# Kernel optimization log

Measured on AMD Instinct MI355X. Metric: run time of the kernel, lower is better.

## Reference

```python
import jax, jax.numpy as jnp
import numpy as np

N_USERS = 50000
N_DISHES = 10000
N_EDGES = 200000
D_IN = 1024
HID = 256
OUT = 128


def _dense_params(key, d_in, d_out):
    kw, kb = jax.random.split(key)
    W = jax.random.normal(kw, (d_in, d_out), jnp.float32) * (1.0 / np.sqrt(d_in))
    b = jnp.zeros((d_out,), jnp.float32)
    return W, b


def setup_inputs() -> dict:
    key = jax.random.key(0)
    ks = jax.random.split(key, 12)
    inp = {
        "user_feat": jax.random.normal(ks[0], (N_USERS, D_IN), jnp.float32),
        "dish_feat": jax.random.normal(ks[1], (N_DISHES, D_IN), jnp.float32),
        "edge_user": jax.random.randint(ks[2], (N_EDGES,), 0, N_USERS, jnp.int32),
        "edge_dish": jax.random.randint(ks[3], (N_EDGES,), 0, N_DISHES, jnp.int32),
    }
    inp["W_ui"], inp["b_ui"] = _dense_params(ks[4], D_IN, HID)   # user_initial_proj
    inp["W_di"], inp["b_di"] = _dense_params(ks[5], D_IN, HID)   # dish_initial_proj
    inp["W_um"], inp["b_um"] = _dense_params(ks[6], D_IN, HID)   # user_message_fn (sender=dish)
    inp["W_dm"], inp["b_dm"] = _dense_params(ks[7], D_IN, HID)   # dish_message_fn (sender=user)
    inp["W_uu"], inp["b_uu"] = _dense_params(ks[8], HID, HID)    # user_update_fn
    inp["W_du"], inp["b_du"] = _dense_params(ks[9], HID, HID)    # dish_update_fn
    inp["W_up"], inp["b_up"] = _dense_params(ks[10], HID, OUT)   # user_proj
    inp["W_dp"], inp["b_dp"] = _dense_params(ks[11], HID, OUT)   # dish_proj
    return inp


def reference(user_feat, dish_feat, edge_user, edge_dish,
              W_ui, b_ui, W_di, b_di, W_um, b_um, W_dm, b_dm,
              W_uu, b_uu, W_du, b_du, W_up, b_up, W_dp, b_dp):
    # initial projections
    user_init = jax.nn.relu(user_feat @ W_ui + b_ui)   # [U, H]
    dish_init = jax.nn.relu(dish_feat @ W_di + b_di)   # [D, H]

    # SimpleConv on 'interacts_reverse': sender=dish, receiver=user
    u_msg = jax.nn.relu(dish_feat[edge_dish] @ W_um + b_um)          # [E, H]
    user_agg = jax.ops.segment_sum(u_msg, edge_user, num_segments=N_USERS)
    user_upd = jax.nn.relu((user_agg + user_init) @ W_uu + b_uu)
    user_emb = user_upd @ W_up + b_up                                 # [U, OUT]

    # SimpleConv on 'interacts': sender=user, receiver=dish
    d_msg = jax.nn.relu(user_feat[edge_user] @ W_dm + b_dm)          # [E, H]
    dish_agg = jax.ops.segment_sum(d_msg, edge_dish, num_segments=N_DISHES)
    dish_upd = jax.nn.relu((dish_agg + dish_init) @ W_du + b_du)
    dish_emb = dish_upd @ W_dp + b_dp                                 # [D, OUT]

    return (user_emb, dish_emb)
```

## Files before the change

### kernel.cpp

```cpp
#include <hip/hip_runtime.h>
#include <hip/hip_bf16.h>

#define D_IN  1024
#define HID   256
#define OUT_D 128

using bf16x8  = __attribute__((ext_vector_type(8))) short;
using bf16x4  = __attribute__((ext_vector_type(4))) short;
using f32x4   = __attribute__((ext_vector_type(4))) float;
typedef unsigned int u32;

__device__ inline float bf2f(short s) {
    unsigned u = ((unsigned)(unsigned short)s) << 16;
    return __uint_as_float(u);
}
__device__ inline short f2bf(float f) {
    __hip_bfloat16 h = __float2bfloat16(f);
    return *reinterpret_cast<short*>(&h);
}

__device__ __forceinline__ void gld16(void* lds, const void* g) {
    __builtin_amdgcn_global_load_lds(
        (const __attribute__((address_space(1))) u32*)g,
        (__attribute__((address_space(3))) u32*)lds, 16, 0, 0);
}

__global__ void pack_all(
    const float* __restrict__ W_ui, const float* __restrict__ W_dm,
    const float* __restrict__ W_di, const float* __restrict__ W_um,
    const float* __restrict__ W_uu, const float* __restrict__ W_du,
    const float* __restrict__ W_up, const float* __restrict__ W_dp,
    const float* __restrict__ b_ui, const float* __restrict__ b_dm,
    const float* __restrict__ b_di, const float* __restrict__ b_um,
    short* __restrict__ Wut, short* __restrict__ Wdt,
    short* __restrict__ Wuut, short* __restrict__ Wdut,
    short* __restrict__ Wupt, short* __restrict__ Wdpt,
    float* __restrict__ bu, float* __restrict__ bd)
{
    const int z = blockIdx.z;
    const int tx = threadIdx.x, ty = threadIdx.y;
    if (z == 8) {
        if (blockIdx.x != 0 || blockIdx.y != 0) return;
        int t = ty * 32 + tx;
        bu[t] = b_ui[t]; bu[256 + t] = b_dm[t];
        bd[t] = b_di[t]; bd[256 + t] = b_um[t];
        return;
    }
    const float* in; short* out; int K, N, n_off = 0;
    switch (z) {
        case 0: in = W_ui; out = Wut;  K = 1024; N = 256; n_off = 0;   break;
        case 1: in = W_dm; out = Wut;  K = 1024; N = 256; n_off = 256; break;
        case 2: in = W_di; out = Wdt;  K = 1024; N = 256; n_off = 0;   break;
        case 3: in = W_um; out = Wdt;  K = 1024; N = 256; n_off = 256; break;
        case 4: in = W_uu; out = Wuut; K = 256;  N = 256; break;
        case 5: in = W_du; out = Wdut; K = 256;  N = 256; break;
        case 6: in = W_up; out = Wupt; K = 256;  N = 128; break;
        default:in = W_dp; out = Wdpt; K = 256;  N = 128; break;
    }
    const int n0 = blockIdx.x * 32, k0 = blockIdx.y * 32;
    if (n0 >= N || k0 >= K) return;
    __shared__ float t[32][33];
#pragma unroll
    for (int j = 0; j < 32; j += 8)
        t[ty + j][tx] = in[(size_t)(k0 + ty + j) * N + (n0 + tx)];
    __syncthreads();
#pragma unroll
    for (int j = 0; j < 32; j += 8)
        out[(size_t)(n_off + n0 + ty + j) * K + (k0 + tx)] = f2bf(t[tx][ty + j]);
}

template <bool RELU, bool AF32, bool CF32>
__global__ __launch_bounds__(256) void mfma_gemm2(
    const void* __restrict__ A0_, int lda0, const short* __restrict__ Wt0,
    const float* __restrict__ bias0, void* __restrict__ C0,
    int M0, int N0, int K0, int nN0, int nb0,
    const void* __restrict__ A1_, int lda1, const short* __restrict__ Wt1,
    const float* __restrict__ bias1, void* __restrict__ C1,
    int M1, int N1, int K1, int nN1)
{
    constexpr int ABYTES = AF32 ? 16384 : 8192;
    constexpr int BBYTES = 8192;
    __shared__ __align__(16) char smem[ABYTES + BBYTES];
    char* As = smem;
    char* Bs = smem + ABYTES;

    const int tid = threadIdx.x;

    const void* A_; const short* Wt; const float* bias; void* Cv;
    int lda, M, N, K, nN, nwg, orig;
    if ((int)blockIdx.x < nb0) {
        A_ = A0_; lda = lda0; Wt = Wt0; bias = bias0; Cv = C0;
        M = M0; N = N0; K = K0; nN = nN0; nwg = nb0; orig = blockIdx.x;
    } else {
        A_ = A1_; lda = lda1; Wt = Wt1; bias = bias1; Cv = C1;
        M = M1; N = N1; K = K1; nN = nN1;
        nwg = gridDim.x - nb0; orig = blockIdx.x - nb0;
    }

    const int qq = nwg >> 3, rr = nwg & 7;
    const int xcd = orig & 7, pos = orig >> 3;
    const int wg = (xcd < rr) ? (xcd * (qq + 1) + pos)
                              : (rr * (qq + 1) + (xcd - rr) * qq + pos);
    const int n0 = (wg % nN) * 128;
    const int m0 = (wg / nN) * 128;

    const int w = tid >> 6, l = tid & 63;
    const int wm = (w >> 1) * 64, wn = (w & 1) * 64;
    const int fr = l & 15, fg = l >> 4;

    f32x4 acc[4][4] = {};

    const char* Ab = (const char*)A_;
    const char* Bb = (const char*)Wt;
    const size_t lda_b = (size_t)lda * (AF32 ? 4 : 2);
    const size_t ldb_b = (size_t)K * 2;

    for (int k0 = 0; k0 < K; k0 += 32) {
        if constexpr (AF32) {
#pragma unroll
            for (int i = 0; i < 4; ++i) {
                int o = i * 4096 + tid * 16;
                int row = o >> 7, cb = o & 127;
                int scb = cb ^ ((row & 7) << 4);
                int arow = m0 + row; if (arow > M - 1) arow = M - 1;
                gld16(As + o, Ab + (size_t)arow * lda_b + (size_t)k0 * 4 + scb);
            }
        } else {
#pragma unroll
            for (int i = 0; i < 2; ++i) {
                int o = i * 4096 + tid * 16;
                int row = o >> 6, cb = o & 63;
                int scb = cb ^ ((row & 3) << 4);
                int arow = m0 + row; if (arow > M - 1) arow = M - 1;
                gld16(As + o, Ab + (size_t)arow * lda_b + (size_t)k0 * 2 + scb);
            }
        }
#pragma unroll
        for (int i = 0; i < 2; ++i) {
            int o = i * 4096 + tid * 16;
            int row = o >> 6, cb = o & 63;
            int scb = cb ^ ((row & 3) << 4);
            gld16(Bs + o, Bb + (size_t)(n0 + row) * ldb_b + (size_t)k0 * 2 + scb);
        }
        __syncthreads();

        bf16x8 af[4], bfv[4];
#pragma unroll
        for (int i = 0; i < 4; ++i) {
            int row = wm + i * 16 + fr;
            if constexpr (AF32) {
                int sw = (row & 7) << 4;
                const char* rb = As + row * 128;
                f32x4 lo = *reinterpret_cast<const f32x4*>(rb + ((fg * 32) ^ sw));
                f32x4 hi = *reinterpret_cast<const f32x4*>(rb + ((fg * 32 + 16) ^ sw));
                bf16x8 t;
                t[0] = f2bf(lo[0]); t[1] = f2bf(lo[1]);
                t[2] = f2bf(lo[2]); t[3] = f2bf(lo[3]);
                t[4] = f2bf(hi[0]); t[5] = f2bf(hi[1]);
                t[6] = f2bf(hi[2]); t[7] = f2bf(hi[3]);
                af[i] = t;
            } else {
                int cb = (fg * 16) ^ ((row & 3) << 4);
                af[i] = *reinterpret_cast<const bf16x8*>(As + row * 64 + cb);
            }
        }
#pragma unroll
        for (int j = 0; j < 4; ++j) {
            int row = wn + j * 16 + fr;
            int cb = (fg * 16) ^ ((row & 3) << 4);
            bfv[j] = *reinterpret_cast<const bf16x8*>(Bs + row * 64 + cb);
        }
#pragma unroll
        for (int i = 0; i < 4; ++i)
#pragma unroll
            for (int j = 0; j < 4; ++j)
                acc[i][j] = __builtin_amdgcn_mfma_f32_16x16x32_bf16(
                    af[i], bfv[j], acc[i][j], 0, 0, 0);

        __syncthreads();
    }

#pragma unroll
    for (int i = 0; i < 4; ++i) {
#pragma unroll
        for (int e = 0; e < 4; ++e) {
            int gm = m0 + wm + i * 16 + fg * 4 + e;
            if (gm >= M) continue;
#pragma unroll
            for (int j = 0; j < 4; ++j) {
                int gn = n0 + wn + j * 16 + fr;
                float v = acc[i][j][e] + bias[gn];
                if (RELU) v = fmaxf(v, 0.f);
                if (CF32) ((float*)Cv)[(size_t)gm * N + gn] = v;
                else      ((short*)Cv)[(size_t)gm * N + gn] = f2bf(v);
            }
        }
    }
}

__global__ void hist2(const int* __restrict__ eu, const int* __restrict__ ed,
                      int* __restrict__ cu, int* __restrict__ cd, int E)
{
    int i = blockIdx.x * blockDim.x + threadIdx.x;
    if (i < E) atomicAdd(&cu[eu[i]], 1);
    else if (i < 2 * E) atomicAdd(&cd[ed[i - E]], 1);
}

__global__ __launch_bounds__(1024) void scan2(
    const int* __restrict__ cnt_u, int* __restrict__ offs_u, int U,
    const int* __restrict__ cnt_d, int* __restrict__ offs_d, int D)
{
    const int* cnt = (blockIdx.x == 0) ? cnt_u : cnt_d;
    int* offs      = (blockIdx.x == 0) ? offs_u : offs_d;
    const int n    = (blockIdx.x == 0) ? U : D;

    __shared__ int tsum[1024];
    const int t = threadIdx.x;
    const int chunk = (n + 1023) / 1024;
    const int lo = t * chunk;
    const int hi = min(lo + chunk, n);
    int s = 0;
    for (int i = lo; i < hi; ++i) s += cnt[i];
    tsum[t] = s;
    __syncthreads();
    for (int d = 1; d < 1024; d <<= 1) {
        int v = (t >= d) ? tsum[t - d] : 0;
        __syncthreads();
        tsum[t] += v;
        __syncthreads();
    }
    int run = (t > 0) ? tsum[t - 1] : 0;
    for (int i = lo; i < hi; ++i) {
        offs[i] = run;
        run += cnt[i];
    }
}

__global__ void fill2(const int* __restrict__ eu, const int* __restrict__ ed,
                      int* __restrict__ offs_u, int* __restrict__ srcl_u,
                      int* __restrict__ offs_d, int* __restrict__ srcl_d, int E)
{
    int i = blockIdx.x * blockDim.x + threadIdx.x;
    if (i < E) {
        int p = atomicAdd(&offs_u[eu[i]], 1);
        srcl_u[p] = ed[i];
    } else if (i < 2 * E) {
        int k = i - E;
        int p = atomicAdd(&offs_d[ed[k]], 1);
        srcl_d[p] = eu[k];
    }
}

__global__ __launch_bounds__(256) void seg_sum_both(
    const short* __restrict__ dish_msg, const short* __restrict__ user_msg,
    const int* __restrict__ srcl_u, const int* __restrict__ offs_u,
    const int* __restrict__ cnt_u,
    const int* __restrict__ srcl_d, const int* __restrict__ offs_d,
    const int* __restrict__ cnt_d,
    short* __restrict__ user_buf, short* __restrict__ dish_buf,
    int U, int D, int nbU)
{
    const short* msg; const int *sl, *oe, *ct; short* acc; int nRows, rb;
    if (blockIdx.x < nbU) {
        msg = dish_msg; sl = srcl_u; oe = offs_u; ct = cnt_u;
        acc = user_buf; nRows = U; rb = blockIdx.x;
    } else {
        msg = user_msg; sl = srcl_d; oe = offs_d; ct = cnt_d;
        acc = dish_buf; nRows = D; rb = blockIdx.x - nbU;
    }
    int row = rb * 4 + (threadIdx.x >> 6);
    if (row >= nRows) return;
    const int lane = threadIdx.x & 63;
    const int deg = ct[row];
    if (deg == 0) return;
    const int base = oe[row] - deg;

    float s0 = 0.f, s1 = 0.f, s2 = 0.f, s3 = 0.f;
    int j = 0;
    for (; j + 4 <= deg; j += 4) {
        int i0 = sl[base + j], i1 = sl[base + j + 1];
        int i2 = sl[base + j + 2], i3 = sl[base + j + 3];
        bf16x4 v0 = *(const bf16x4*)&msg[(size_t)i0 * 512 + lane * 4];
        bf16x4 v1 = *(const bf16x4*)&msg[(size_t)i1 * 512 + lane * 4];
        bf16x4 v2 = *(const bf16x4*)&msg[(size_t)i2 * 512 + lane * 4];
        bf16x4 v3 = *(const bf16x4*)&msg[(size_t)i3 * 512 + lane * 4];
        s0 += bf2f(v0[0]) + bf2f(v1[0]) + bf2f(v2[0]) + bf2f(v3[0]);
        s1 += bf2f(v0[1]) + bf2f(v1[1]) + bf2f(v2[1]) + bf2f(v3[1]);
        s2 += bf2f(v0[2]) + bf2f(v1[2]) + bf2f(v2[2]) + bf2f(v3[2]);
        s3 += bf2f(v0[3]) + bf2f(v1[3]) + bf2f(v2[3]) + bf2f(v3[3]);
    }
    for (; j < deg; ++j) {
        int i0 = sl[base + j];
        bf16x4 v = *(const bf16x4*)&msg[(size_t)i0 * 512 + lane * 4];
        s0 += bf2f(v[0]); s1 += bf2f(v[1]); s2 += bf2f(v[2]); s3 += bf2f(v[3]);
    }
    bf16x4 c = *(bf16x4*)&acc[(size_t)row * 512 + lane * 4];
    c[0] = f2bf(bf2f(c[0]) + s0);
    c[1] = f2bf(bf2f(c[1]) + s1);
    c[2] = f2bf(bf2f(c[2]) + s2);
    c[3] = f2bf(bf2f(c[3]) + s3);
    *(bf16x4*)&acc[(size_t)row * 512 + lane * 4] = c;
}

extern "C" void kernel_launch(void* const* d_in, const int* in_sizes, int n_in,
                              void* d_out, int out_size, void* d_ws, size_t ws_size,
                              hipStream_t stream)
{
    const float* user_feat = (const float*)d_in[0];
    const float* dish_feat = (const float*)d_in[1];
    const int*   edge_user = (const int*)d_in[2];
    const int*   edge_dish = (const int*)d_in[3];
    const float* W_ui = (const float*)d_in[4];  const float* b_ui = (const float*)d_in[5];
    const float* W_di = (const float*)d_in[6];  const float* b_di = (const float*)d_in[7];
    const float* W_um = (const float*)d_in[8];  const float* b_um = (const float*)d_in[9];
    const float* W_dm = (const float*)d_in[10]; const float* b_dm = (const float*)d_in[11];
    const float* W_uu = (const float*)d_in[12]; const float* b_uu = (const float*)d_in[13];
    const float* W_du = (const float*)d_in[14]; const float* b_du = (const float*)d_in[15];
    const float* W_up = (const float*)d_in[16]; const float* b_up = (const float*)d_in[17];
    const float* W_dp = (const float*)d_in[18]; const float* b_dp = (const float*)d_in[19];

    const int U = in_sizes[0] / D_IN;
    const int D = in_sizes[1] / D_IN;
    const int E = in_sizes[2];

    float* out = (float*)d_out;
    float* user_emb = out;
    float* dish_emb = out + (size_t)U * OUT_D;

    short* sws = (short*)d_ws;
    short* user_buf = sws;
    short* dish_buf = user_buf + (size_t)U * 512;
    short* user_upd = dish_buf + (size_t)D * 512;
    short* dish_upd = user_upd + (size_t)U * 256;
    short* Wut  = dish_upd + (size_t)D * 256;
    short* Wdt  = Wut  + (size_t)512 * 1024;
    short* Wuut = Wdt  + (size_t)512 * 1024;
    short* Wdut = Wuut + (size_t)256 * 256;
    short* Wupt = Wdut + (size_t)256 * 256;
    short* Wdpt = Wupt + (size_t)128 * 256;
    float* bu   = (float*)(Wdpt + (size_t)128 * 256);
    float* bd   = bu + 512;
    int*   cnt_u  = (int*)(bd + 512);
    int*   cnt_d  = cnt_u + U;
    int*   offs_u = cnt_d + D;
    int*   offs_d = offs_u + U;
    int*   srcl_u = offs_d + D;
    int*   srcl_d = srcl_u + E;

    hipLaunchKernelGGL(pack_all, dim3(8, 32, 9), dim3(32, 8), 0, stream,
                       W_ui, W_dm, W_di, W_um, W_uu, W_du, W_up, W_dp,
                       b_ui, b_dm, b_di, b_um,
                       Wut, Wdt, Wuut, Wdut, Wupt, Wdpt, bu, bd);

    hipMemsetAsync(cnt_u, 0, (size_t)(U + D) * sizeof(int), stream);
    int eg2 = (2 * E + 255) / 256;
    hipLaunchKernelGGL(hist2, dim3(eg2), dim3(256), 0, stream,
                       edge_user, edge_dish, cnt_u, cnt_d, E);
    hipLaunchKernelGGL(scan2, dim3(2), dim3(1024), 0, stream,
                       cnt_u, offs_u, U, cnt_d, offs_d, D);
    hipLaunchKernelGGL(fill2, dim3(eg2), dim3(256), 0, stream,
                       edge_user, edge_dish, offs_u, srcl_u, offs_d, srcl_d, E);

    const int nbU128 = (U + 127) / 128;
    const int nbD128 = (D + 127) / 128;

    {
        int nb0 = nbU128 * 4, nb1 = nbD128 * 4;
        hipLaunchKernelGGL((mfma_gemm2<true, true, false>),
                           dim3(nb0 + nb1), dim3(256), 0, stream,
                           user_feat, D_IN, Wut, bu, user_buf, U, 512, D_IN, 4, nb0,
                           dish_feat, D_IN, Wdt, bd, dish_buf, D, 512, D_IN, 4);
    }

    int nbU = (U + 3) / 4;
    hipLaunchKernelGGL(seg_sum_both, dim3(nbU + (D + 3) / 4), dim3(256), 0, stream,
                       dish_buf + HID, user_buf + HID,
                       srcl_u, offs_u, cnt_u, srcl_d, offs_d, cnt_d,
                       user_buf, dish_buf, U, D, nbU);

    {
        int nb0 = nbU128 * 2, nb1 = nbD128 * 2;
        hipLaunchKernelGGL((mfma_gemm2<true, false, false>),
                           dim3(nb0 + nb1), dim3(256), 0, stream,
                           user_buf, 512, Wuut, b_uu, user_upd, U, HID, HID, 2, nb0,
                           dish_buf, 512, Wdut, b_du, dish_upd, D, HID, HID, 2);
    }

    {
        int nb0 = nbU128, nb1 = nbD128;
        hipLaunchKernelGGL((mfma_gemm2<false, false, true>),
                           dim3(nb0 + nb1), dim3(256), 0, stream,
                           user_upd, HID, Wupt, b_up, user_emb, U, OUT_D, HID, 1, nb0,
                           dish_upd, HID, Wdpt, b_dp, dish_emb, D, OUT_D, HID, 1);
    }
}
```

Measured before the change: 353.2 us.

## Triple-buffer GEMM LDS tiles with async prefetch two k-steps ahead

Turns the single-buffered LDS staging in the fused MFMA GEMM into a three-stage ring. Global-to-LDS loads for step t+2 are issued before step t is computed, and explicit vmcnt waits plus raw barriers replace the full __syncthreads. The goal is to hide global load latency behind the MFMA work. In exchange LDS use triples (up to 72KB in the fp32-A variant), which can lower occupancy, and the hand-set vmcnt counts depend on the exact number of loads per stage.

Result: no change. 349.7 us (-1.0%).

```diff
diff --git a/kernel.cpp b/kernel.cpp
--- a/kernel.cpp
+++ b/kernel.cpp
@@ -80,9 +80,8 @@
 {
     constexpr int ABYTES = AF32 ? 16384 : 8192;
     constexpr int BBYTES = 8192;
-    __shared__ __align__(16) char smem[ABYTES + BBYTES];
-    char* As = smem;
-    char* Bs = smem + ABYTES;
+    constexpr int STEP = ABYTES + BBYTES;
+    __shared__ __align__(16) char smem[3 * STEP];
 
     const int tid = threadIdx.x;
 
@@ -115,7 +114,9 @@
     const size_t lda_b = (size_t)lda * (AF32 ? 4 : 2);
     const size_t ldb_b = (size_t)K * 2;
 
-    for (int k0 = 0; k0 < K; k0 += 32) {
+    auto stage = [&](int buf, int k0) {
+        char* As = smem + buf * STEP;
+        char* Bs = As + ABYTES;
         if constexpr (AF32) {
 #pragma unroll
             for (int i = 0; i < 4; ++i) {
@@ -142,8 +143,33 @@
             int scb = cb ^ ((row & 3) << 4);
             gld16(Bs + o, Bb + (size_t)(n0 + row) * ldb_b + (size_t)k0 * 2 + scb);
         }
-        __syncthreads();
-
+    };
+
+    const int T = K / 32;
+
+    stage(0, 0);
+    stage(1, 32);
+
+    int bsel = 0;
+    for (int t = 0; t < T; ++t) {
+        if (t + 2 < T) {
+            int nb2 = bsel + 2; if (nb2 >= 3) nb2 -= 3;
+            stage(nb2, (t + 2) * 32);
+            __builtin_amdgcn_sched_barrier(0);
+            if constexpr (AF32) asm volatile("s_waitcnt vmcnt(12)" ::: "memory");
+            else                asm volatile("s_waitcnt vmcnt(8)"  ::: "memory");
+        } else if (t + 1 < T) {
+            if constexpr (AF32) asm volatile("s_waitcnt vmcnt(6)" ::: "memory");
+            else                asm volatile("s_waitcnt vmcnt(4)" ::: "memory");
+        } else {
+            asm volatile("s_waitcnt vmcnt(0)" ::: "memory");
+        }
+        __builtin_amdgcn_sched_barrier(0);
+        __builtin_amdgcn_s_barrier();
+        __builtin_amdgcn_sched_barrier(0);
+
+        const char* As = smem + bsel * STEP;
+        const char* Bs = As + ABYTES;
         bf16x8 af[4], bfv[4];
 #pragma unroll
         for (int i = 0; i < 4; ++i) {
@@ -153,12 +179,12 @@
                 const char* rb = As + row * 128;
                 f32x4 lo = *reinterpret_cast<const f32x4*>(rb + ((fg * 32) ^ sw));
                 f32x4 hi = *reinterpret_cast<const f32x4*>(rb + ((fg * 32 + 16) ^ sw));
-                bf16x8 t;
-                t[0] = f2bf(lo[0]); t[1] = f2bf(lo[1]);
-                t[2] = f2bf(lo[2]); t[3] = f2bf(lo[3]);
-                t[4] = f2bf(hi[0]); t[5] = f2bf(hi[1]);
-                t[6] = f2bf(hi[2]); t[7] = f2bf(hi[3]);
-                af[i] = t;
+                bf16x8 tt;
+                tt[0] = f2bf(lo[0]); tt[1] = f2bf(lo[1]);
+                tt[2] = f2bf(lo[2]); tt[3] = f2bf(lo[3]);
+                tt[4] = f2bf(hi[0]); tt[5] = f2bf(hi[1]);
+                tt[6] = f2bf(hi[2]); tt[7] = f2bf(hi[3]);
+                af[i] = tt;
             } else {
                 int cb = (fg * 16) ^ ((row & 3) << 4);
                 af[i] = *reinterpret_cast<const bf16x8*>(As + row * 64 + cb);
@@ -177,7 +203,11 @@
                 acc[i][j] = __builtin_amdgcn_mfma_f32_16x16x32_bf16(
                     af[i], bfv[j], acc[i][j], 0, 0, 0);
 
-        __syncthreads();
+        __builtin_amdgcn_sched_barrier(0);
+        __builtin_amdgcn_s_barrier();
+        __builtin_amdgcn_sched_barrier(0);
+
+        bsel = (bsel == 2) ? 0 : bsel + 1;
     }
 
 #pragma unroll
```

## Double GEMM K-step to 64 and write segment sums to compact buffers

Applied to the files above, without the earlier changes.

The GEMM main loop now stages 64 K-columns per iteration instead of 32, with larger LDS tiles and an 8-row XOR swizzle, and runs two MFMA sub-steps between barriers. This halves the barrier and load-issue overhead per tile. The segment-sum kernel now writes init+agg into separate compact 256-wide buffers, so the update GEMM reads contiguous rows with lda 256 instead of strided 512-wide rows, and zero-degree rows are written too. The cost is double the LDS per block, which may lower occupancy, plus extra workspace for the compact buffers.

Measured after the change: 329.3 us. 1.07x faster.

```diff
diff --git a/kernel.cpp b/kernel.cpp
--- a/kernel.cpp
+++ b/kernel.cpp
@@ -78,8 +78,8 @@
     const float* __restrict__ bias1, void* __restrict__ C1,
     int M1, int N1, int K1, int nN1)
 {
-    constexpr int ABYTES = AF32 ? 16384 : 8192;
-    constexpr int BBYTES = 8192;
+    constexpr int ABYTES = AF32 ? 32768 : 16384;
+    constexpr int BBYTES = 16384;
     __shared__ __align__(16) char smem[ABYTES + BBYTES];
     char* As = smem;
     char* Bs = smem + ABYTES;
@@ -115,68 +115,71 @@
     const size_t lda_b = (size_t)lda * (AF32 ? 4 : 2);
     const size_t ldb_b = (size_t)K * 2;
 
-    for (int k0 = 0; k0 < K; k0 += 32) {
+    for (int k0 = 0; k0 < K; k0 += 64) {
         if constexpr (AF32) {
+#pragma unroll
+            for (int i = 0; i < 8; ++i) {
+                int o = i * 4096 + tid * 16;
+                int row = o >> 8, cb = o & 255;
+                int scb = cb ^ ((row & 7) << 4);
+                int arow = m0 + row; if (arow > M - 1) arow = M - 1;
+                gld16(As + o, Ab + (size_t)arow * lda_b + (size_t)k0 * 4 + scb);
+            }
+        } else {
 #pragma unroll
             for (int i = 0; i < 4; ++i) {
                 int o = i * 4096 + tid * 16;
                 int row = o >> 7, cb = o & 127;
                 int scb = cb ^ ((row & 7) << 4);
                 int arow = m0 + row; if (arow > M - 1) arow = M - 1;
-                gld16(As + o, Ab + (size_t)arow * lda_b + (size_t)k0 * 4 + scb);
-            }
-        } else {
-#pragma unroll
-            for (int i = 0; i < 2; ++i) {
-                int o = i * 4096 + tid * 16;
-                int row = o >> 6, cb = o & 63;
-                int scb = cb ^ ((row & 3) << 4);
-                int arow = m0 + row; if (arow > M - 1) arow = M - 1;
                 gld16(As + o, Ab + (size_t)arow * lda_b + (size_t)k0 * 2 + scb);
             }
         }
 #pragma unroll
-        for (int i = 0; i < 2; ++i) {
+        for (int i = 0; i < 4; ++i) {
             int o = i * 4096 + tid * 16;
-            int row = o >> 6, cb = o & 63;
-            int scb = cb ^ ((row & 3) << 4);
+            int row = o >> 7, cb = o & 127;
+            int scb = cb ^ ((row & 7) << 4);
             gld16(Bs + o, Bb + (size_t)(n0 + row) * ldb_b + (size_t)k0 * 2 + scb);
         }
         __syncthreads();
 
-        bf16x8 af[4], bfv[4];
-#pragma unroll
-        for (int i = 0; i < 4; ++i) {
-            int row = wm + i * 16 + fr;
-            if constexpr (AF32) {
+#pragma unroll
+        for (int kk = 0; kk < 2; ++kk) {
+            bf16x8 af[4], bfv[4];
+#pragma unroll
+            for (int i = 0; i < 4; ++i) {
+                int row = wm + i * 16 + fr;
                 int sw = (row & 7) << 4;
-                const char* rb = As + row * 128;
-                f32x4 lo = *reinterpret_cast<const f32x4*>(rb + ((fg * 32) ^ sw));
-                f32x4 hi = *reinterpret_cast<const f32x4*>(rb + ((fg * 32 + 16) ^ sw));
-                bf16x8 t;
-                t[0] = f2bf(lo[0]); t[1] = f2bf(lo[1]);
-                t[2] = f2bf(lo[2]); t[3] = f2bf(lo[3]);
-                t[4] = f2bf(hi[0]); t[5] = f2bf(hi[1]);
-                t[6] = f2bf(hi[2]); t[7] = f2bf(hi[3]);
-                af[i] = t;
-            } else {
-                int cb = (fg * 16) ^ ((row & 3) << 4);
-                af[i] = *reinterpret_cast<const bf16x8*>(As + row * 64 + cb);
+                if constexpr (AF32) {
+                    int cbase = kk * 128 + fg * 32;
+                    const char* rb = As + row * 256;
+                    f32x4 lo = *reinterpret_cast<const f32x4*>(rb + (cbase ^ sw));
+                    f32x4 hi = *reinterpret_cast<const f32x4*>(rb + ((cbase + 16) ^ sw));
+                    bf16x8 t;
+                    t[0] = f2bf(lo[0]); t[1] = f2bf(lo[1]);
+                    t[2] = f2bf(lo[2]); t[3] = f2bf(lo[3]);
+                    t[4] = f2bf(hi[0]); t[5] = f2bf(hi[1]);
+                    t[6] = f2bf(hi[2]); t[7] = f2bf(hi[3]);
+                    af[i] = t;
+                } else {
+                    int cb = (kk * 64 + fg * 16) ^ sw;
+                    af[i] = *reinterpret_cast<const bf16x8*>(As + row * 128 + cb);
+                }
             }
+#pragma unroll
+            for (int j = 0; j < 4; ++j) {
+                int row = wn + j * 16 + fr;
+                int cb = (kk * 64 + fg * 16) ^ ((row & 7) << 4);
+                bfv[j] = *reinterpret_cast<const bf16x8*>(Bs + row * 128 + cb);
+            }
+#pragma unroll
+            for (int i = 0; i < 4; ++i)
+#pragma unroll
+                for (int j = 0; j < 4; ++j)
+                    acc[i][j] = __builtin_amdgcn_mfma_f32_16x16x32_bf16(
+                        af[i], bfv[j], acc[i][j], 0, 0, 0);
         }
-#pragma unroll
-        for (int j = 0; j < 4; ++j) {
-            int row = wn + j * 16 + fr;
-            int cb = (fg * 16) ^ ((row & 3) << 4);
-            bfv[j] = *reinterpret_cast<const bf16x8*>(Bs + row * 64 + cb);
-        }
-#pragma unroll
-        for (int i = 0; i < 4; ++i)
-#pragma unroll
-            for (int j = 0; j < 4; ++j)
-                acc[i][j] = __builtin_amdgcn_mfma_f32_16x16x32_bf16(
-                    af[i], bfv[j], acc[i][j], 0, 0, 0);
-
         __syncthreads();
     }
 
@@ -257,22 +260,23 @@
     const int* __restrict__ cnt_u,
     const int* __restrict__ srcl_d, const int* __restrict__ offs_d,
     const int* __restrict__ cnt_d,
-    short* __restrict__ user_buf, short* __restrict__ dish_buf,
+    const short* __restrict__ user_init, const short* __restrict__ dish_init,
+    short* __restrict__ user_cmp, short* __restrict__ dish_cmp,
     int U, int D, int nbU)
 {
-    const short* msg; const int *sl, *oe, *ct; short* acc; int nRows, rb;
+    const short* msg; const short* init_; const int *sl, *oe, *ct;
+    short* outp; int nRows, rb;
     if (blockIdx.x < nbU) {
         msg = dish_msg; sl = srcl_u; oe = offs_u; ct = cnt_u;
-        acc = user_buf; nRows = U; rb = blockIdx.x;
+        init_ = user_init; outp = user_cmp; nRows = U; rb = blockIdx.x;
     } else {
         msg = user_msg; sl = srcl_d; oe = offs_d; ct = cnt_d;
-        acc = dish_buf; nRows = D; rb = blockIdx.x - nbU;
+        init_ = dish_init; outp = dish_cmp; nRows = D; rb = blockIdx.x - nbU;
     }
     int row = rb * 4 + (threadIdx.x >> 6);
     if (row >= nRows) return;
     const int lane = threadIdx.x & 63;
     const int deg = ct[row];
-    if (deg == 0) return;
     const int base = oe[row] - deg;
 
     float s0 = 0.f, s1 = 0.f, s2 = 0.f, s3 = 0.f;
@@ -294,12 +298,13 @@
         bf16x4 v = *(const bf16x4*)&msg[(size_t)i0 * 512 + lane * 4];
         s0 += bf2f(v[0]); s1 += bf2f(v[1]); s2 += bf2f(v[2]); s3 += bf2f(v[3]);
     }
-    bf16x4 c = *(bf16x4*)&acc[(size_t)row * 512 + lane * 4];
-    c[0] = f2bf(bf2f(c[0]) + s0);
-    c[1] = f2bf(bf2f(c[1]) + s1);
-    c[2] = f2bf(bf2f(c[2]) + s2);
-    c[3] = f2bf(bf2f(c[3]) + s3);
-    *(bf16x4*)&acc[(size_t)row * 512 + lane * 4] = c;
+    bf16x4 c = *(const bf16x4*)&init_[(size_t)row * 512 + lane * 4];
+    bf16x4 o;
+    o[0] = f2bf(bf2f(c[0]) + s0);
+    o[1] = f2bf(bf2f(c[1]) + s1);
+    o[2] = f2bf(bf2f(c[2]) + s2);
+    o[3] = f2bf(bf2f(c[3]) + s3);
+    *(bf16x4*)&outp[(size_t)row * 256 + lane * 4] = o;
 }
 
 extern "C" void kernel_launch(void* const* d_in, const int* in_sizes, int n_in,
@@ -330,7 +335,9 @@
     short* sws = (short*)d_ws;
     short* user_buf = sws;
     short* dish_buf = user_buf + (size_t)U * 512;
-    short* user_upd = dish_buf + (size_t)D * 512;
+    short* user_cmp = dish_buf + (size_t)D * 512;
+    short* dish_cmp = user_cmp + (size_t)U * 256;
+    short* user_upd = dish_cmp + (size_t)D * 256;
     short* dish_upd = user_upd + (size_t)U * 256;
     short* Wut  = dish_upd + (size_t)D * 256;
     short* Wdt  = Wut  + (size_t)512 * 1024;
@@ -376,14 +383,14 @@
     hipLaunchKernelGGL(seg_sum_both, dim3(nbU + (D + 3) / 4), dim3(256), 0, stream,
                        dish_buf + HID, user_buf + HID,
                        srcl_u, offs_u, cnt_u, srcl_d, offs_d, cnt_d,
-                       user_buf, dish_buf, U, D, nbU);
+                       user_buf, dish_buf, user_cmp, dish_cmp, U, D, nbU);
 
     {
         int nb0 = nbU128 * 2, nb1 = nbD128 * 2;
         hipLaunchKernelGGL((mfma_gemm2<true, false, false>),
                            dim3(nb0 + nb1), dim3(256), 0, stream,
-                           user_buf, 512, Wuut, b_uu, user_upd, U, HID, HID, 2, nb0,
-                           dish_buf, 512, Wdut, b_du, dish_upd, D, HID, HID, 2);
+                           user_cmp, 256, Wuut, b_uu, user_upd, U, HID, HID, 2, nb0,
+                           dish_cmp, 256, Wdut, b_du, dish_upd, D, HID, HID, 2);
     }
 
     {
```
